# Kernel optimization log

Measured on AMD Instinct MI355X. Metric: run time of the kernel, lower is better.

The kernel has to match this reference:

```python
import jax, jax.numpy as jnp
import numpy as np

HID = 2048; S = 2048; NH = 16
Q_LORA = 1536; KV_LORA = 512
D_NOPE = 128; D_ROPE = 64; D_V = 128
D_QK = D_NOPE + D_ROPE  # 192
EPS = 1e-6


def setup_inputs() -> dict:
    key = jax.random.key(0)
    ks = jax.random.split(key, 8)
    hidden_states = jax.random.normal(ks[0], (1, S, HID), dtype=jnp.float32)
    # real RoPE tables, HF layout: cos/sin = concat(freqs, freqs) along last dim
    inv_freq = 1.0 / (10000.0 ** (np.arange(0, D_ROPE, 2, dtype=np.float32) / D_ROPE))
    t = np.arange(S, dtype=np.float32)
    freqs = np.outer(t, inv_freq)  # [S, D_ROPE//2]
    emb = np.concatenate([freqs, freqs], axis=-1)  # [S, D_ROPE]
    cos = jnp.asarray(np.cos(emb))[None]  # [1, S, D_ROPE]
    sin = jnp.asarray(np.sin(emb))[None]
    def lin(k, fan_in, fan_out):
        return jax.random.normal(k, (fan_in, fan_out), dtype=jnp.float32) / np.sqrt(fan_in)
    return {
        'hidden_states': hidden_states, 'cos': cos, 'sin': sin,
        'w_qa': lin(ks[1], HID, Q_LORA),
        'g_qa': jnp.ones((Q_LORA,), jnp.float32),
        'w_qb': lin(ks[2], Q_LORA, NH * D_QK),
        'w_kva': lin(ks[3], HID, KV_LORA + D_ROPE),
        'g_kva': jnp.ones((KV_LORA,), jnp.float32),
        'w_kvb': lin(ks[4], KV_LORA, NH * (D_NOPE + D_V)),
        'w_o': lin(ks[5], NH * D_V, HID),
    }


def _rmsnorm(x, g):
    var = jnp.mean(x * x, axis=-1, keepdims=True)
    return x * jax.lax.rsqrt(var + EPS) * g


def _deinterleave(x):
    # view (..., d//2, 2) -> transpose -> reshape: even-index dims first, then odd
    b, h, s, d = x.shape
    return x.reshape(b, h, s, d // 2, 2).transpose(0, 1, 2, 4, 3).reshape(b, h, s, d)


def _rotate_half(x):
    x1, x2 = jnp.split(x, 2, axis=-1)
    return jnp.concatenate([-x2, x1], axis=-1)


def _apply_rope(q, k, cos, sin):
    cos = cos[:, None]  # [B,1,S,D]
    sin = sin[:, None]
    q = _deinterleave(q)
    k = _deinterleave(k)
    q_emb = q * cos + _rotate_half(q) * sin
    k_emb = k * cos + _rotate_half(k) * sin
    return q_emb, k_emb


def reference(hidden_states, cos, sin, w_qa, g_qa, w_qb, w_kva, g_kva, w_kvb, w_o):
    bsz, q_len, _ = hidden_states.shape
    # low-rank Q projection
    q = _rmsnorm(hidden_states @ w_qa, g_qa) @ w_qb  # [B,S,NH*D_QK]
    q = q.reshape(bsz, q_len, NH, D_QK).transpose(0, 2, 1, 3)  # [B,NH,S,D_QK]
    q_nope, q_pe = q[..., :D_NOPE], q[..., D_NOPE:]
    # compressed KV + shared rope key
    ckv = hidden_states @ w_kva  # [B,S,KV_LORA+D_ROPE]
    compressed_kv, k_pe = ckv[..., :KV_LORA], ckv[..., KV_LORA:]
    k_pe = k_pe.reshape(bsz, q_len, 1, D_ROPE).transpose(0, 2, 1, 3)  # [B,1,S,D_ROPE]
    kv = (_rmsnorm(compressed_kv, g_kva) @ w_kvb).reshape(bsz, q_len, NH, D_NOPE + D_V).transpose(0, 2, 1, 3)
    k_nope, value_states = kv[..., :D_NOPE], kv[..., D_NOPE:]
    # interleaved RoPE
    q_pe, k_pe = _apply_rope(q_pe, k_pe, cos, sin)
    query_states = jnp.concatenate([q_nope, q_pe], axis=-1)  # [B,NH,S,D_QK]
    key_states = jnp.concatenate([k_nope, jnp.broadcast_to(k_pe, (bsz, NH, q_len, D_ROPE))], axis=-1)
    # causal attention with MLA softmax scale
    scale = D_QK ** (-0.5)
    scores = jnp.einsum('bhqd,bhkd->bhqk', query_states, key_states) * scale
    mask = jnp.tril(jnp.ones((q_len, q_len), dtype=bool))
    scores = jnp.where(mask, scores, jnp.finfo(scores.dtype).min)
    probs = jax.nn.softmax(scores, axis=-1)
    attn = jnp.einsum('bhqk,bhkd->bhqd', probs, value_states)  # [B,NH,S,D_V]
    attn = attn.transpose(0, 2, 1, 3).reshape(bsz, q_len, NH * D_V)
    return attn @ w_o
```

## Files before the change

kernel.cpp:

```cpp
#include <hip/hip_runtime.h>
#include <hip/hip_bf16.h>

#define S_LEN 2048
#define HID_D 2048
#define NHEAD 16
#define QLORA 1536
#define KVLORA 512
#define DNOPE 128
#define DROPE 64
#define DV 128
#define DQK 192
#define CKV_PAD 640

#define KS_SH (64 * 192)
#define VS_SH (128 * 64)
#define BUF_SH (KS_SH + VS_SH)

typedef __hip_bfloat16 bf16;
typedef __attribute__((ext_vector_type(8))) short short8;
typedef __attribute__((ext_vector_type(4))) short s16x4;
typedef __attribute__((ext_vector_type(4))) float f32x4;

__device__ __forceinline__ float ldE(const float* p) { return *p; }
__device__ __forceinline__ float ldE(const bf16* p) { return __bfloat162float(*p); }
__device__ __forceinline__ void stE(float* p, float v) { *p = v; }
__device__ __forceinline__ void stE(bf16* p, float v) { *p = __float2bfloat16(v); }

__device__ __forceinline__ short bf16bits(float v) {
    __hip_bfloat16 h = __float2bfloat16(v);
    return *reinterpret_cast<short*>(&h);
}

__device__ __forceinline__ float b2f(short s) {
    union { short s; bf16 h; } u;
    u.s = s;
    return __bfloat162float(u.h);
}

__device__ __forceinline__ f32x4 mfma16(short8 a, short8 b, f32x4 c) {
    return __builtin_amdgcn_mfma_f32_16x16x32_bf16(a, b, c, 0, 0, 0);
}

__device__ __forceinline__ void gload16(const void* g, void* l) {
    __builtin_amdgcn_global_load_lds(
        (const __attribute__((address_space(1))) unsigned int*)g,
        (__attribute__((address_space(3))) unsigned int*)l, 16, 0, 0);
}

__global__ void detect_kernel(const void* hidden, int* flag) {
    __shared__ int red[256];
    const int tid = threadIdx.x;
    const bf16* hb = (const bf16*)hidden;
    float a = fabsf(__bfloat162float(hb[tid]));
    red[tid] = (!(a < 64.f) || (a != 0.f && a < 1e-30f)) ? 1 : 0;
    __syncthreads();
    for (int o = 128; o > 0; o >>= 1) {
        if (tid < o) red[tid] += red[tid + o];
        __syncthreads();
    }
    if (tid == 0) *flag = (red[0] > 16) ? 1 : 0;
}

__global__ void convert_kernel(const void* in, bf16* out, int n8, const int* flag) {
    int i = blockIdx.x * 256 + threadIdx.x;
    if (i >= n8) return;
    size_t off = (size_t)i * 8;
    short8 o;
    if (*flag) {
        const float* f = (const float*)in + off;
#pragma unroll
        for (int j = 0; j < 8; ++j) o[j] = bf16bits(f[j]);
    } else {
        o = *(const short8*)((const short*)in + off);
    }
    *(short8*)((short*)out + off) = o;
}

__global__ void transpose_kernel(const void* in, bf16* out, int K, int N, int Npad,
                                 const int* flag) {
    __shared__ __align__(16) short Ts[64][80];
    const int tid = threadIdx.x;
    const int n0 = blockIdx.x * 64, k0 = blockIdx.y * 64;
    const bool inb = n0 < N;
    const int fp32 = *flag;
    const int kl = tid >> 4;
    const int nl = (tid & 15) * 4;
#pragma unroll
    for (int p = 0; p < 4; ++p) {
        int k = kl + p * 16;
        float v[4] = {0.f, 0.f, 0.f, 0.f};
        if (inb) {
            if (fp32) {
                const float4 f = *(const float4*)((const float*)in + (size_t)(k0 + k) * N + n0 + nl);
                v[0] = f.x; v[1] = f.y; v[2] = f.z; v[3] = f.w;
            } else {
                const bf16* bp = (const bf16*)in + (size_t)(k0 + k) * N + n0 + nl;
#pragma unroll
                for (int i = 0; i < 4; ++i) v[i] = __bfloat162float(bp[i]);
            }
        }
#pragma unroll
        for (int i = 0; i < 4; ++i) Ts[nl + i][k] = bf16bits(v[i]);
    }
    __syncthreads();
    const int nr = tid >> 2;
    const int kq = (tid & 3) * 16;
    short* op = (short*)out + (size_t)(n0 + nr) * K + k0 + kq;
    *(short8*)op = *(short8*)&Ts[nr][kq];
    *(short8*)(op + 8) = *(short8*)&Ts[nr][kq + 8];
}

template <int MODE, typename TC>
__device__ void mgemm_body(const bf16* __restrict__ A, const bf16* __restrict__ Bt,
                           TC* __restrict__ C, int M, int N, int K,
                           bf16* __restrict__ Kn, bf16* __restrict__ Vt) {
    __shared__ __align__(16) short As[128 * 32];
    __shared__ __align__(16) short Bs[128 * 32];
    const int tid = threadIdx.x;
    const int w = tid >> 6, lane = tid & 63;
    const int lg = lane >> 4, ln = lane & 15;
    const int wm = w >> 1, wn = w & 1;
    const int m0 = blockIdx.y * 128, n0 = blockIdx.x * 128;

    const int c0 = w * 128 + lane, c1 = c0 + 64;
    const int r0 = c0 >> 2, kq0 = (c0 & 3) ^ ((r0 >> 1) & 3);
    const int r1 = c1 >> 2, kq1 = (c1 & 3) ^ ((r1 >> 1) & 3);
    const bf16* aP0 = A + (size_t)(m0 + r0) * K + kq0 * 8;
    const bf16* aP1 = A + (size_t)(m0 + r1) * K + kq1 * 8;
    const bf16* bP0 = Bt + (size_t)(n0 + r0) * K + kq0 * 8;
    const bf16* bP1 = Bt + (size_t)(n0 + r1) * K + kq1 * 8;
    short* aL0 = As + (size_t)(w * 128) * 8;
    short* aL1 = As + (size_t)(w * 128 + 64) * 8;
    short* bL0 = Bs + (size_t)(w * 128) * 8;
    short* bL1 = Bs + (size_t)(w * 128 + 64) * 8;

    const int sx = lg ^ ((ln >> 1) & 3);
    int aoff[4], boff[4];
#pragma unroll
    for (int i = 0; i < 4; ++i) {
        aoff[i] = (wm * 64 + i * 16 + ln) * 32 + sx * 8;
        boff[i] = (wn * 64 + i * 16 + ln) * 32 + sx * 8;
    }

    f32x4 acc[4][4];
#pragma unroll
    for (int i = 0; i < 4; ++i)
#pragma unroll
        for (int j = 0; j < 4; ++j) acc[i][j] = (f32x4){0.f, 0.f, 0.f, 0.f};

    for (int k0 = 0; k0 < K; k0 += 32) {
        __syncthreads();
        gload16(aP0 + k0, aL0);
        gload16(aP1 + k0, aL1);
        gload16(bP0 + k0, bL0);
        gload16(bP1 + k0, bL1);
        __syncthreads();
        short8 af[4], bfr[4];
#pragma unroll
        for (int i = 0; i < 4; ++i) af[i] = *(const short8*)&As[aoff[i]];
#pragma unroll
        for (int j = 0; j < 4; ++j) bfr[j] = *(const short8*)&Bs[boff[j]];
#pragma unroll
        for (int i = 0; i < 4; ++i)
#pragma unroll
            for (int j = 0; j < 4; ++j) acc[i][j] = mfma16(af[i], bfr[j], acc[i][j]);
    }
    if constexpr (MODE == 2) {
#pragma unroll
        for (int i = 0; i < 4; ++i)
#pragma unroll
            for (int j = 0; j < 4; ++j) {
                const int col = n0 + wn * 64 + j * 16 + ln;
                const int row = m0 + wm * 64 + i * 16 + lg * 4;
                const int h = col >> 8, d = col & 255;
                if (d < DNOPE) {
                    bf16* cp = Kn + (size_t)row * (NHEAD * DNOPE) + h * DNOPE + d;
#pragma unroll
                    for (int r = 0; r < 4; ++r)
                        cp[(size_t)r * (NHEAD * DNOPE)] = __float2bfloat16(acc[i][j][r]);
                } else {
                    s16x4 pk;
#pragma unroll
                    for (int r = 0; r < 4; ++r) pk[r] = bf16bits(acc[i][j][r]);
                    *(s16x4*)(Vt + (size_t)(h * DV + (d - DNOPE)) * S_LEN + row) = pk;
                }
            }
    } else {
#pragma unroll
        for (int i = 0; i < 4; ++i)
#pragma unroll
            for (int j = 0; j < 4; ++j) {
                TC* cp = C + (size_t)(m0 + wm * 64 + i * 16 + lg * 4) * N + n0 + wn * 64 + j * 16 + ln;
#pragma unroll
                for (int r = 0; r < 4; ++r)
                    stE(cp + (size_t)r * N, acc[i][j][r]);
            }
    }
}

template <int MODE>
__global__ __launch_bounds__(256, 2)
void mgemm_kernel(const bf16* A, const bf16* Bt, void* C, int M, int N, int K,
                  const int* flag, bf16* Kn, bf16* Vt) {
    if (MODE == 1 && *flag) mgemm_body<1, float>(A, Bt, (float*)C, M, N, K, nullptr, nullptr);
    else if (MODE == 2)     mgemm_body<2, bf16>(A, Bt, (bf16*)C, M, N, K, Kn, Vt);
    else                    mgemm_body<0, bf16>(A, Bt, (bf16*)C, M, N, K, nullptr, nullptr);
}

template <typename TG>
__device__ void rmsnorm_body(const bf16* __restrict__ x, const TG* __restrict__ g,
                             bf16* __restrict__ y, int len, int xstride, int ystride) {
    const int s = blockIdx.x;
    const int tid = threadIdx.x;
    const bf16* xr = x + (size_t)s * xstride;
    float ss = 0.f;
    for (int i = tid; i < len; i += 256) {
        float v = __bfloat162float(xr[i]);
        ss += v * v;
    }
    __shared__ float red[256];
    red[tid] = ss;
    __syncthreads();
    for (int o = 128; o > 0; o >>= 1) {
        if (tid < o) red[tid] += red[tid + o];
        __syncthreads();
    }
    const float scale = rsqrtf(red[0] / (float)len + 1e-6f);
    bf16* yr = y + (size_t)s * ystride;
    for (int i = tid; i < len; i += 256)
        yr[i] = __float2bfloat16(__bfloat162float(xr[i]) * scale * ldE(&g[i]));
}

__global__ void rmsnorm_kernel(const bf16* x, const void* g, bf16* y,
                               int len, int xstride, int ystride, const int* flag) {
    if (*flag) rmsnorm_body<float>(x, (const float*)g, y, len, xstride, ystride);
    else       rmsnorm_body<bf16>(x, (const bf16*)g, y, len, xstride, ystride);
}

template <typename TG>
__device__ void rope_body(bf16* __restrict__ q, const bf16* __restrict__ ckv,
                          bf16* __restrict__ kpe, const TG* __restrict__ cosb,
                          const TG* __restrict__ sinb) {
    const int s = blockIdx.x;
    const int tid = threadIdx.x;
    float x0 = 0.f, x1 = 0.f, c = 0.f, sn = 0.f;
    bf16* qbase = nullptr;
    int p = 0;
    const bool isq = tid < 512;
    const bool active = tid < 544;
    if (active) {
        if (isq) {
            const int h = tid >> 5;
            p = tid & 31;
            qbase = q + (size_t)s * (NHEAD * DQK) + h * DQK + DNOPE;
            x0 = __bfloat162float(qbase[2 * p]);
            x1 = __bfloat162float(qbase[2 * p + 1]);
        } else {
            p = tid - 512;
            const bf16* kb = ckv + (size_t)s * CKV_PAD + KVLORA;
            x0 = __bfloat162float(kb[2 * p]);
            x1 = __bfloat162float(kb[2 * p + 1]);
        }
        c = ldE(&cosb[s * 64 + p]);
        sn = ldE(&sinb[s * 64 + p]);
    }
    __syncthreads();
    if (active) {
        if (isq) {
            qbase[p] = __float2bfloat16(x0 * c - x1 * sn);
            qbase[p + 32] = __float2bfloat16(x1 * c + x0 * sn);
        } else {
            kpe[s * 64 + p] = __float2bfloat16(x0 * c - x1 * sn);
            kpe[s * 64 + p + 32] = __float2bfloat16(x1 * c + x0 * sn);
        }
    }
}

__global__ void rope_kernel(bf16* q, const bf16* ckv, bf16* kpe,
                            const void* cosb, const void* sinb, const int* flag) {
    if (*flag) rope_body<float>(q, ckv, kpe, (const float*)cosb, (const float*)sinb);
    else       rope_body<bf16>(q, ckv, kpe, (const bf16*)cosb, (const bf16*)sinb);
}

__global__ __launch_bounds__(256, 2)
void fattn_kernel(const bf16* __restrict__ q, const bf16* __restrict__ kn,
                  const bf16* __restrict__ vt, const bf16* __restrict__ kpe,
                  bf16* __restrict__ attn, bf16* __restrict__ Opart, float* __restrict__ ml) {
    const int nf = blockIdx.x;
    const int xcd = nf & 7;
    const int j = nf >> 3;
    const int bx = j & 31;
    const int h = (j >> 5) * 8 + xcd;
    int qt, part, nparts;
    if (bx < 15)      { qt = 15 - bx / 3;        part = bx % 3;        nparts = 3; }
    else if (bx < 27) { qt = 10 - (bx - 15) / 2; part = (bx - 15) & 1; nparts = 2; }
    else              { qt = 31 - bx;            part = 0;             nparts = 1; }
    const int nt = 2 * qt + 2;
    const int bsz = nt / nparts, rr = nt % nparts;
    const int t0 = part * bsz + (part < rr ? part : rr);
    const int t1 = t0 + bsz + (part < rr ? 1 : 0);
    const int q0 = qt * 128;

    const int tid = threadIdx.x;
    const int w = tid >> 6;
    const int l = tid & 63;
    const int lg = l >> 4;
    const int ln = l & 15;

    __shared__ __align__(16) short KV[BUF_SH];
    short* Ks = &KV[0];
    short* Vs = &KV[KS_SH];

    int offK[6], sK[6];
    bool isn[6];
#pragma unroll
    for (int p = 0; p < 6; ++p) {
        const int cid = tid + p * 256;
        const int row = cid / 24;
        const int cpos = cid % 24;
        const int c = (cpos & 24) | ((cpos & 7) ^ (row & 7));
        if (c < 16) {
            offK[p] = row * (NHEAD * DNOPE) + h * DNOPE + c * 8;
            sK[p] = NHEAD * DNOPE;
            isn[p] = true;
        } else {
            offK[p] = row * DROPE + (c - 16) * 8;
            sK[p] = DROPE;
            isn[p] = false;
        }
    }
    int offV[4];
#pragma unroll
    for (int p = 0; p < 4; ++p) {
        const int cid = tid + p * 256;
        const int row = cid >> 3;
        const int cc = (cid & 7) ^ (row & 7);
        offV[p] = (h * DV + row) * S_LEN + cc * 8;
    }

    short8 qf[2][6];
#pragma unroll
    for (int i = 0; i < 2; ++i) {
        const short* qrow =
            (const short*)(q + (size_t)(q0 + i * 64 + w * 16 + ln) * (NHEAD * DQK) + h * DQK);
#pragma unroll
        for (int ks = 0; ks < 6; ++ks)
            qf[i][ks] = *(const short8*)(qrow + ks * 32 + lg * 8);
    }

    f32x4 O[2][8];
#pragma unroll
    for (int i = 0; i < 2; ++i)
#pragma unroll
        for (int ct = 0; ct < 8; ++ct) O[i][ct] = (f32x4){0.f, 0.f, 0.f, 0.f};
    float m_[2][4], l_[2][4];
#pragma unroll
    for (int i = 0; i < 2; ++i)
#pragma unroll
        for (int r = 0; r < 4; ++r) { m_[i][r] = -1e30f; l_[i][r] = 0.f; }
    const float scale = 0.07216878364870322f;

    for (int t = t0; t < t1; ++t) {
        const int k0 = t * 64;
        __syncthreads();
#pragma unroll
        for (int p = 0; p < 6; ++p) {
            const bf16* sp = (isn[p] ? kn : kpe) + (size_t)offK[p] + (size_t)k0 * sK[p];
            gload16(sp, Ks + (w + 4 * p) * 512);
        }
#pragma unroll
        for (int p = 0; p < 4; ++p)
            gload16(vt + (size_t)offV[p] + k0, Vs + (w + 4 * p) * 512);
        __syncthreads();

        f32x4 S[2][4];
#pragma unroll
        for (int i = 0; i < 2; ++i)
#pragma unroll
            for (int c = 0; c < 4; ++c) S[i][c] = (f32x4){0.f, 0.f, 0.f, 0.f};
        __builtin_amdgcn_s_setprio(1);
#pragma unroll
        for (int ks = 0; ks < 6; ++ks) {
            const int kch = ks * 4 + lg;
#pragma unroll
            for (int c = 0; c < 4; ++c) {
                short8 kf = *(const short8*)&Ks[(size_t)(c * 16 + ln) * 192 +
                                               (size_t)(kch ^ (ln & 7)) * 8];
                S[0][c] = mfma16(qf[0][ks], kf, S[0][c]);
                S[1][c] = mfma16(qf[1][ks], kf, S[1][c]);
            }
        }
        __builtin_amdgcn_s_setprio(0);

        const int d0 = k0 - q0;
#pragma unroll
        for (int i = 0; i < 2; ++i)
#pragma unroll
            for (int c = 0; c < 4; ++c)
#pragma unroll
                for (int r = 0; r < 4; ++r) {
                    float v = S[i][c][r] * scale;
                    if (d0 > -64 &&
                        (d0 + c * 16 + ln) > (i * 64 + w * 16 + lg * 4 + r)) v = -1e30f;
                    S[i][c][r] = v;
                }

        float alpha[2][4];
#pragma unroll
        for (int i = 0; i < 2; ++i)
#pragma unroll
            for (int r = 0; r < 4; ++r) {
                float mx = fmaxf(fmaxf(S[i][0][r], S[i][1][r]), fmaxf(S[i][2][r], S[i][3][r]));
#pragma unroll
                for (int d = 1; d < 16; d <<= 1) mx = fmaxf(mx, __shfl_xor(mx, d));
                float mn = fmaxf(m_[i][r], mx);
                alpha[i][r] = __expf(m_[i][r] - mn);
                m_[i][r] = mn;
                float rs = 0.f;
#pragma unroll
                for (int c = 0; c < 4; ++c) {
                    float p = __expf(S[i][c][r] - mn);
                    S[i][c][r] = p;
                    rs += p;
                }
#pragma unroll
                for (int d = 1; d < 16; d <<= 1) rs += __shfl_xor(rs, d);
                l_[i][r] = l_[i][r] * alpha[i][r] + rs;
            }
#pragma unroll
        for (int i = 0; i < 2; ++i)
#pragma unroll
            for (int ct = 0; ct < 8; ++ct)
#pragma unroll
                for (int r = 0; r < 4; ++r) O[i][ct][r] *= alpha[i][r];

        __syncthreads();
        short* Pb = Ks;
#pragma unroll
        for (int i = 0; i < 2; ++i)
#pragma unroll
            for (int c = 0; c < 4; ++c)
#pragma unroll
                for (int r = 0; r < 4; ++r)
                    Pb[(size_t)(i * 64 + w * 16 + lg * 4 + r) * 70 + c * 16 + ln] =
                        bf16bits(S[i][c][r]);

        __builtin_amdgcn_s_setprio(1);
#pragma unroll
        for (int ks = 0; ks < 2; ++ks) {
            short8 pf0 = *(const short8*)&Pb[(size_t)(w * 16 + ln) * 70 + ks * 32 + lg * 8];
            short8 pf1 = *(const short8*)&Pb[(size_t)(64 + w * 16 + ln) * 70 + ks * 32 + lg * 8];
#pragma unroll
            for (int ct = 0; ct < 8; ++ct) {
                short8 vf = *(const short8*)&Vs[(size_t)(ct * 16 + ln) * 64 +
                                               (size_t)((ks * 4 + lg) ^ (ln & 7)) * 8];
                O[0][ct] = mfma16(pf0, vf, O[0][ct]);
                O[1][ct] = mfma16(pf1, vf, O[1][ct]);
            }
        }
        __builtin_amdgcn_s_setprio(0);
    }

    if (nparts == 1) {
#pragma unroll
        for (int i = 0; i < 2; ++i)
#pragma unroll
            for (int r = 0; r < 4; ++r) {
                float inv = 1.f / l_[i][r];
                bf16* orow = attn + (size_t)(q0 + i * 64 + w * 16 + lg * 4 + r) * (NHEAD * DV) +
                             h * DV;
#pragma unroll
                for (int ct = 0; ct < 8; ++ct)
                    orow[ct * 16 + ln] = __float2bfloat16(O[i][ct][r] * inv);
            }
    } else {
        const int mlslot = h * 27 + (qt <= 10 ? (qt - 5) * 2 + part : 12 + (qt - 11) * 3 + part);
        float* mlp = ml + (size_t)mlslot * 128 * 2;
        if (part == 0) {
#pragma unroll
            for (int i = 0; i < 2; ++i)
#pragma unroll
                for (int r = 0; r < 4; ++r) {
                    const int rowb = i * 64 + w * 16 + lg * 4 + r;
                    bf16* orow = attn + (size_t)(q0 + rowb) * (NHEAD * DV) + h * DV;
#pragma unroll
                    for (int ct = 0; ct < 8; ++ct)
                        orow[ct * 16 + ln] = __float2bfloat16(O[i][ct][r]);
                    if (ln == 0) {
                        mlp[rowb * 2] = m_[i][r];
                        mlp[rowb * 2 + 1] = l_[i][r];
                    }
                }
        } else {
            const int oslot = h * 16 + (qt <= 10 ? (qt - 5) : 6 + (qt - 11) * 2 + (part - 1));
            bf16* op = Opart + (size_t)oslot * 128 * DV;
#pragma unroll
            for (int i = 0; i < 2; ++i)
#pragma unroll
                for (int r = 0; r < 4; ++r) {
                    const int rowb = i * 64 + w * 16 + lg * 4 + r;
#pragma unroll
                    for (int ct = 0; ct < 8; ++ct)
                        op[(size_t)rowb * DV + ct * 16 + ln] = __float2bfloat16(O[i][ct][r]);
                    if (ln == 0) {
                        mlp[rowb * 2] = m_[i][r];
                        mlp[rowb * 2 + 1] = l_[i][r];
                    }
                }
        }
    }
}

__global__ void reduce_kernel(const bf16* __restrict__ Opart, const float* __restrict__ ml,
                              bf16* __restrict__ attn) {
    const int qq = blockIdx.x;
    const int h = blockIdx.y;
    const int qt = 5 + qq;
    const int np = (qt <= 10) ? 2 : 3;
    const int q0 = qt * 128;
    const int tid = threadIdx.x;
    const int row = tid >> 1;
    const int dh = (tid & 1) * 64;
    float mp[3], lp[3], f[3];
    float mm = -1e30f;
    for (int p = 0; p < np; ++p) {
        const int msl = h * 27 + (qt <= 10 ? (qt - 5) * 2 + p : 12 + (qt - 11) * 3 + p);
        mp[p] = ml[((size_t)msl * 128 + row) * 2];
        lp[p] = ml[((size_t)msl * 128 + row) * 2 + 1];
        mm = fmaxf(mm, mp[p]);
    }
    float denom = 0.f;
    for (int p = 0; p < np; ++p) {
        f[p] = __expf(mp[p] - mm);
        denom += f[p] * lp[p];
    }
    const float inv = 1.f / denom;
    const int os1 = h * 16 + (qt <= 10 ? (qt - 5) : 6 + (qt - 11) * 2);
    bf16* arow = attn + (size_t)(q0 + row) * (NHEAD * DV) + h * DV + dh;
    const bf16* o1 = Opart + ((size_t)os1 * 128 + row) * DV + dh;
    const bf16* o2 = o1 + (size_t)128 * DV;
#pragma unroll
    for (int jc = 0; jc < 8; ++jc) {
        short8 a = *(const short8*)(arow + jc * 8);
        short8 b1 = *(const short8*)(o1 + jc * 8);
        short8 b2 = (np == 3) ? *(const short8*)(o2 + jc * 8) : b1;
        short8 o;
#pragma unroll
        for (int e = 0; e < 8; ++e) {
            float v = f[0] * b2f(a[e]) + f[1] * b2f(b1[e]);
            if (np == 3) v += f[2] * b2f(b2[e]);
            o[e] = bf16bits(v * inv);
        }
        *(short8*)(arow + jc * 8) = o;
    }
}

extern "C" void kernel_launch(void* const* d_in, const int* in_sizes, int n_in,
                              void* d_out, int out_size, void* d_ws, size_t ws_size,
                              hipStream_t stream) {
    const void* hidden = d_in[0];
    const void* cosb   = d_in[1];
    const void* sinb   = d_in[2];
    const void* w_qa   = d_in[3];
    const void* g_qa   = d_in[4];
    const void* w_qb   = d_in[5];
    const void* w_kva  = d_in[6];
    const void* g_kva  = d_in[7];
    const void* w_kvb  = d_in[8];
    const void* w_o    = d_in[9];

    bf16* ws = (bf16*)d_ws;
    bf16* q_a  = ws;
    bf16* ckv  = q_a + (size_t)S_LEN * QLORA;
    bf16* ckvn = ckv + (size_t)S_LEN * CKV_PAD;
    bf16* q    = ckvn + (size_t)S_LEN * KVLORA;
    bf16* kn   = q + (size_t)S_LEN * NHEAD * DQK;
    bf16* vtb  = kn + (size_t)S_LEN * NHEAD * DNOPE;
    bf16* kpe  = vtb + (size_t)NHEAD * DV * S_LEN;
    bf16* hbf  = kpe + (size_t)S_LEN * DROPE;
    int* flag  = (int*)(hbf + (size_t)S_LEN * HID_D);
    bf16* attn = ws;
    float* ml  = (float*)(ws + (size_t)S_LEN * HID_D);
    bf16* Opart = hbf;
    bf16* W01  = kn;
    bf16* W23  = q_a;
    bf16* W4   = q;

    detect_kernel<<<1, 256, 0, stream>>>(hidden, flag);
    convert_kernel<<<(S_LEN * HID_D / 8 + 255) / 256, 256, 0, stream>>>(
        hidden, hbf, S_LEN * HID_D / 8, flag);

    transpose_kernel<<<dim3(QLORA / 64, HID_D / 64), 256, 0, stream>>>(
        w_qa, W01, HID_D, QLORA, QLORA, flag);
    mgemm_kernel<0><<<dim3(QLORA / 128, S_LEN / 128), 256, 0, stream>>>(
        hbf, W01, q_a, S_LEN, QLORA, HID_D, flag, nullptr, nullptr);
    rmsnorm_kernel<<<S_LEN, 256, 0, stream>>>(q_a, g_qa, q_a, QLORA, QLORA, QLORA, flag);
    transpose_kernel<<<dim3(NHEAD * DQK / 64, QLORA / 64), 256, 0, stream>>>(
        w_qb, W01, QLORA, NHEAD * DQK, NHEAD * DQK, flag);
    mgemm_kernel<0><<<dim3(NHEAD * DQK / 128, S_LEN / 128), 256, 0, stream>>>(
        q_a, W01, q, S_LEN, NHEAD * DQK, QLORA, flag, nullptr, nullptr);
    transpose_kernel<<<dim3(CKV_PAD / 64, HID_D / 64), 256, 0, stream>>>(
        w_kva, W23, HID_D, KVLORA + DROPE, CKV_PAD, flag);
    mgemm_kernel<0><<<dim3(CKV_PAD / 128, S_LEN / 128), 256, 0, stream>>>(
        hbf, W23, ckv, S_LEN, CKV_PAD, HID_D, flag, nullptr, nullptr);
    rmsnorm_kernel<<<S_LEN, 256, 0, stream>>>(ckv, g_kva, ckvn, KVLORA, CKV_PAD, KVLORA, flag);
    transpose_kernel<<<dim3(NHEAD * (DNOPE + DV) / 64, KVLORA / 64), 256, 0, stream>>>(
        w_kvb, W23, KVLORA, NHEAD * (DNOPE + DV), NHEAD * (DNOPE + DV), flag);
    mgemm_kernel<2><<<dim3(NHEAD * (DNOPE + DV) / 128, S_LEN / 128), 256, 0, stream>>>(
        ckvn, W23, kn, S_LEN, NHEAD * (DNOPE + DV), KVLORA, flag, kn, vtb);
    rope_kernel<<<S_LEN, 576, 0, stream>>>(q, ckv, kpe, cosb, sinb, flag);
    fattn_kernel<<<dim3(512), 256, 0, stream>>>(q, kn, vtb, kpe, attn, Opart, ml);
    reduce_kernel<<<dim3(11, NHEAD), 256, 0, stream>>>(Opart, ml, attn);
    transpose_kernel<<<dim3(HID_D / 64, HID_D / 64), 256, 0, stream>>>(
        w_o, W4, HID_D, HID_D, HID_D, flag);
    mgemm_kernel<1><<<dim3(HID_D / 128, S_LEN / 128), 256, 0, stream>>>(
        attn, W4, d_out, S_LEN, HID_D, HID_D, flag, nullptr, nullptr);
}
```

Baseline: 408.3 us.

## Double-buffer K/V tiles in attention loop to overlap global loads with compute

The single shared K/V buffer becomes two ping-pong buffers. The first tile is loaded before the loop, and each iteration issues the loads for the next tile before computing on the current one. A partial vmcnt wait replaces the old full __syncthreads pair, so global-to-LDS traffic overlaps the QK and PV MFMA work. This doubles the LDS per block, which may reduce how many blocks fit on a CU. It also adds a barrier at the end of each iteration to protect buffer reuse.

Result: no change. 408.4 us (+0.0%).

```diff
diff --git a/kernel.cpp b/kernel.cpp
--- a/kernel.cpp
+++ b/kernel.cpp
@@ -307,9 +307,7 @@
     const int lg = l >> 4;
     const int ln = l & 15;
 
-    __shared__ __align__(16) short KV[BUF_SH];
-    short* Ks = &KV[0];
-    short* Vs = &KV[KS_SH];
+    __shared__ __align__(16) short KV[2][BUF_SH];
 
     int offK[6], sK[6];
     bool isn[6];
@@ -360,19 +358,41 @@
         for (int r = 0; r < 4; ++r) { m_[i][r] = -1e30f; l_[i][r] = 0.f; }
     const float scale = 0.07216878364870322f;
 
-    for (int t = t0; t < t1; ++t) {
-        const int k0 = t * 64;
-        __syncthreads();
+    {
+        const int k0 = t0 * 64;
 #pragma unroll
         for (int p = 0; p < 6; ++p) {
             const bf16* sp = (isn[p] ? kn : kpe) + (size_t)offK[p] + (size_t)k0 * sK[p];
-            gload16(sp, Ks + (w + 4 * p) * 512);
+            gload16(sp, &KV[0][0] + (w + 4 * p) * 512);
         }
 #pragma unroll
         for (int p = 0; p < 4; ++p)
-            gload16(vt + (size_t)offV[p] + k0, Vs + (w + 4 * p) * 512);
-        __syncthreads();
-
+            gload16(vt + (size_t)offV[p] + k0, &KV[0][KS_SH] + (w + 4 * p) * 512);
+    }
+
+    for (int t = t0; t < t1; ++t) {
+        const int cur = (t - t0) & 1;
+        short* Ks = &KV[cur][0];
+        short* Vs = &KV[cur][KS_SH];
+        if (t + 1 < t1) {
+            const int k0n = (t + 1) * 64;
+            short* KsN = &KV[cur ^ 1][0];
+            short* VsN = &KV[cur ^ 1][KS_SH];
+#pragma unroll
+            for (int p = 0; p < 6; ++p) {
+                const bf16* sp = (isn[p] ? kn : kpe) + (size_t)offK[p] + (size_t)k0n * sK[p];
+                gload16(sp, KsN + (w + 4 * p) * 512);
+            }
+#pragma unroll
+            for (int p = 0; p < 4; ++p)
+                gload16(vt + (size_t)offV[p] + k0n, VsN + (w + 4 * p) * 512);
+            asm volatile("s_waitcnt vmcnt(10)" ::: "memory");
+        } else {
+            asm volatile("s_waitcnt vmcnt(0)" ::: "memory");
+        }
+        __builtin_amdgcn_s_barrier();
+
+        const int k0 = t * 64;
         f32x4 S[2][4];
 #pragma unroll
         for (int i = 0; i < 2; ++i)
@@ -434,7 +454,7 @@
 #pragma unroll
                 for (int r = 0; r < 4; ++r) O[i][ct][r] *= alpha[i][r];
 
-        __syncthreads();
+        __builtin_amdgcn_s_barrier();
         short* Pb = Ks;
 #pragma unroll
         for (int i = 0; i < 2; ++i)
@@ -459,6 +479,7 @@
             }
         }
         __builtin_amdgcn_s_setprio(0);
+        __builtin_amdgcn_s_barrier();
     }
 
     if (nparts == 1) {
```
